# Kernel optimization log

Measured on AMD Instinct MI355X. Metric: run time of the kernel, lower is better.

The kernel has to match this reference:

```python
import jax, jax.numpy as jnp
import numpy as np

N, D_IN, D_HID, P, D_OUT = 131072, 256, 256, 256, 2


def setup_inputs() -> dict:
    key = jax.random.key(0)
    ks = jax.random.split(key, 10)
    s_in = 1.0 / np.sqrt(D_IN)
    s_h = 1.0 / np.sqrt(D_HID)
    s_o = 1.0 / np.sqrt(P)
    return {
        "X_batch": jax.random.normal(ks[0], (N, D_IN), dtype=jnp.float32),
        "W_in": jax.random.uniform(ks[1], (D_HID, D_IN), jnp.float32, -s_in, s_in),
        "b_in": jax.random.uniform(ks[2], (D_HID,), jnp.float32, -s_in, s_in),
        "W_h1": jax.random.uniform(ks[3], (D_HID, D_HID), jnp.float32, -s_h, s_h),
        "b_h1": jax.random.uniform(ks[4], (D_HID,), jnp.float32, -s_h, s_h),
        "W_h2": jax.random.uniform(ks[5], (D_HID, D_HID), jnp.float32, -s_h, s_h),
        "b_h2": jax.random.uniform(ks[6], (D_HID,), jnp.float32, -s_h, s_h),
        "prototype": jax.random.normal(ks[7], (P, D_HID), dtype=jnp.float32),
        "W_out": jax.random.uniform(ks[8], (D_OUT, P), jnp.float32, -s_o, s_o),
        "b_out": jax.random.uniform(ks[9], (D_OUT,), jnp.float32, -s_o, s_o),
        "assignment": 0,
    }


def reference(X_batch, W_in, b_in, W_h1, b_h1, W_h2, b_h2, prototype, W_out, b_out, assignment):
    # forward_a: fc_in + relu, then hidden layers + relu
    h = jax.nn.relu(X_batch @ W_in.T + b_in)          # (N, d)
    h = jax.nn.relu(h @ W_h1.T + b_h1)
    h = jax.nn.relu(h @ W_h2.T + b_h2)
    # forward_prototype: L2-normalize hidden and prototypes, then inner product.
    hn = h / jnp.linalg.norm(h, axis=1, keepdims=True)                      # (N, d)
    pn = prototype / jnp.linalg.norm(prototype, axis=1, keepdims=True)      # (p, d)
    # FAITHFUL to torch: .view(1, d, p) is a row-major RESHAPE of (p, d),
    # not a transpose. The broadcast mul+sum reduces to a single GEMM.
    d, p = hn.shape[1], pn.shape[0]
    proto_mat = pn.reshape(d, p)                                            # (d, p)
    inner = hn @ proto_mat                                                  # (N, p)
    return inner @ W_out.T + b_out                                          # (N, out)
```

## Files before the change

kernel.cpp:

```cpp
#include <hip/hip_runtime.h>
#include <hip/hip_bf16.h>

#define DHID 256
#define ROWS 64
#define THREADS 512
#define NROWS 131072

typedef __attribute__((ext_vector_type(8))) __bf16 bf16x8;
typedef __attribute__((ext_vector_type(4))) float f32x4;

__device__ __forceinline__ unsigned short f2b(float f) {
    union { float f; unsigned u; } x; x.f = f;
    unsigned r = x.u + 0x7fffu + ((x.u >> 16) & 1u);
    return (unsigned short)(r >> 16);
}

__device__ __forceinline__ int hswz(int row, int col) {
    return ((row << 9) + (col << 1)) ^ ((row & 7) << 4);
}

__global__ void conv_w(const float* __restrict__ w0, const float* __restrict__ w1,
                       const float* __restrict__ w2, unsigned short* __restrict__ out) {
    int i = blockIdx.x * blockDim.x + threadIdx.x;
    const float* src = (i < 65536) ? w0 : (i < 131072 ? w1 : w2);
    int rem  = i & 65535;
    int e    = rem & 7;
    int lane = (rem >> 3) & 63;
    int blk  = rem >> 9;
    int kk   = blk & 7;
    int c16  = blk >> 3;
    int row  = c16 * 16 + (lane & 15);
    int col  = kk * 32 + 8 * (lane >> 4) + e;
    out[i] = f2b(src[row * 256 + col]);
}

__global__ void make_m(const float* __restrict__ proto, const float* __restrict__ wout,
                       float2* __restrict__ M) {
    int k = blockIdx.x;
    int l = threadIdx.x;
    float s2 = 0.f, d0 = 0.f, d1 = 0.f;
#pragma unroll
    for (int q = 0; q < 4; ++q) {
        int c = l + 64 * q;
        float p = proto[k * 256 + c];
        s2 += p * p;
        d0 += p * wout[c];
        d1 += p * wout[256 + c];
    }
#pragma unroll
    for (int off = 32; off; off >>= 1) {
        s2 += __shfl_xor(s2, off);
        d0 += __shfl_xor(d0, off);
        d1 += __shfl_xor(d1, off);
    }
    if (l == 0) {
        float rinv = rsqrtf(s2);
        M[k] = make_float2(d0 * rinv, d1 * rinv);
    }
}

__device__ __forceinline__ void layer(const unsigned short* hin, unsigned short* hout,
                                      const unsigned short* W, const float* __restrict__ bias,
                                      int lane, int wave) {
    const int l15 = lane & 15;
    const int g   = lane >> 4;
    const int jw  = wave * 32;

    f32x4 acc[4][2];
#pragma unroll
    for (int ci = 0; ci < 2; ++ci) {
        const float4 bv = *reinterpret_cast<const float4*>(&bias[jw + 16 * ci + 4 * g]);
#pragma unroll
        for (int ri = 0; ri < 4; ++ri) {
            acc[ri][ci][0] = bv.x; acc[ri][ci][1] = bv.y;
            acc[ri][ci][2] = bv.z; acc[ri][ci][3] = bv.w;
        }
    }

    const char* hin_b = reinterpret_cast<const char*>(hin);
    const unsigned short* wp[2];
#pragma unroll
    for (int ci = 0; ci < 2; ++ci)
        wp[ci] = W + ((wave * 2 + ci) * 8) * 512 + lane * 8;

    bf16x8 bcur[2];
#pragma unroll
    for (int ci = 0; ci < 2; ++ci) bcur[ci] = *reinterpret_cast<const bf16x8*>(wp[ci]);

#pragma unroll
    for (int kk = 0; kk < 8; ++kk) {
        const int k0 = kk * 32 + 8 * g;
        bf16x8 a[4];
#pragma unroll
        for (int ri = 0; ri < 4; ++ri)
            a[ri] = *reinterpret_cast<const bf16x8*>(hin_b + hswz(16 * ri + l15, k0));
        bf16x8 bnxt[2];
        if (kk < 7) {
#pragma unroll
            for (int ci = 0; ci < 2; ++ci)
                bnxt[ci] = *reinterpret_cast<const bf16x8*>(wp[ci] + (kk + 1) * 512);
        }
#pragma unroll
        for (int ri = 0; ri < 4; ++ri)
#pragma unroll
            for (int ci = 0; ci < 2; ++ci)
                acc[ri][ci] = __builtin_amdgcn_mfma_f32_16x16x32_bf16(bcur[ci], a[ri], acc[ri][ci], 0, 0, 0);
        if (kk < 7) { bcur[0] = bnxt[0]; bcur[1] = bnxt[1]; }
    }

    char* hout_b = reinterpret_cast<char*>(hout);
#pragma unroll
    for (int ri = 0; ri < 4; ++ri) {
        const int row = 16 * ri + l15;
#pragma unroll
        for (int ci = 0; ci < 2; ++ci) {
            const int colb = jw + 16 * ci + 4 * g;
            unsigned long long pk =
                  (unsigned long long)f2b(fmaxf(acc[ri][ci][0], 0.f))
                | ((unsigned long long)f2b(fmaxf(acc[ri][ci][1], 0.f)) << 16)
                | ((unsigned long long)f2b(fmaxf(acc[ri][ci][2], 0.f)) << 32)
                | ((unsigned long long)f2b(fmaxf(acc[ri][ci][3], 0.f)) << 48);
            *reinterpret_cast<unsigned long long*>(hout_b + hswz(row, colb)) = pk;
        }
    }
}

__device__ __forceinline__ void layer3_reduce(const unsigned short* hin,
                                              const unsigned short* W,
                                              const float* __restrict__ bias,
                                              const float2* __restrict__ M,
                                              float* part, int lane, int wave) {
    const int l15 = lane & 15;
    const int g   = lane >> 4;
    const int jw  = wave * 32;

    f32x4 acc[4][2];
#pragma unroll
    for (int ci = 0; ci < 2; ++ci) {
        const float4 bv = *reinterpret_cast<const float4*>(&bias[jw + 16 * ci + 4 * g]);
#pragma unroll
        for (int ri = 0; ri < 4; ++ri) {
            acc[ri][ci][0] = bv.x; acc[ri][ci][1] = bv.y;
            acc[ri][ci][2] = bv.z; acc[ri][ci][3] = bv.w;
        }
    }

    const char* hin_b = reinterpret_cast<const char*>(hin);
    const unsigned short* wp[2];
#pragma unroll
    for (int ci = 0; ci < 2; ++ci)
        wp[ci] = W + ((wave * 2 + ci) * 8) * 512 + lane * 8;

    bf16x8 bcur[2];
#pragma unroll
    for (int ci = 0; ci < 2; ++ci) bcur[ci] = *reinterpret_cast<const bf16x8*>(wp[ci]);

#pragma unroll
    for (int kk = 0; kk < 8; ++kk) {
        const int k0 = kk * 32 + 8 * g;
        bf16x8 a[4];
#pragma unroll
        for (int ri = 0; ri < 4; ++ri)
            a[ri] = *reinterpret_cast<const bf16x8*>(hin_b + hswz(16 * ri + l15, k0));
        bf16x8 bnxt[2];
        if (kk < 7) {
#pragma unroll
            for (int ci = 0; ci < 2; ++ci)
                bnxt[ci] = *reinterpret_cast<const bf16x8*>(wp[ci] + (kk + 1) * 512);
        }
#pragma unroll
        for (int ri = 0; ri < 4; ++ri)
#pragma unroll
            for (int ci = 0; ci < 2; ++ci)
                acc[ri][ci] = __builtin_amdgcn_mfma_f32_16x16x32_bf16(bcur[ci], a[ri], acc[ri][ci], 0, 0, 0);
        if (kk < 7) { bcur[0] = bnxt[0]; bcur[1] = bnxt[1]; }
    }

    float2 m[2][4];
#pragma unroll
    for (int ci = 0; ci < 2; ++ci)
#pragma unroll
        for (int e = 0; e < 4; ++e)
            m[ci][e] = M[jw + 16 * ci + 4 * g + e];

    float s2[4], d0[4], d1[4];
#pragma unroll
    for (int ri = 0; ri < 4; ++ri) {
        s2[ri] = 0.f; d0[ri] = 0.f; d1[ri] = 0.f;
#pragma unroll
        for (int ci = 0; ci < 2; ++ci)
#pragma unroll
            for (int e = 0; e < 4; ++e) {
                float h = fmaxf(acc[ri][ci][e], 0.f);
                s2[ri] += h * h;
                d0[ri] += h * m[ci][e].x;
                d1[ri] += h * m[ci][e].y;
            }
    }
#pragma unroll
    for (int ri = 0; ri < 4; ++ri) {
        s2[ri] += __shfl_xor(s2[ri], 16); s2[ri] += __shfl_xor(s2[ri], 32);
        d0[ri] += __shfl_xor(d0[ri], 16); d0[ri] += __shfl_xor(d0[ri], 32);
        d1[ri] += __shfl_xor(d1[ri], 16); d1[ri] += __shfl_xor(d1[ri], 32);
    }
    if (lane < 16) {
#pragma unroll
        for (int ri = 0; ri < 4; ++ri) {
            int r = 16 * ri + l15;
            part[r * 8 + wave]        = s2[ri];
            part[512 + r * 8 + wave]  = d0[ri];
            part[1024 + r * 8 + wave] = d1[ri];
        }
    }
}

__global__ __launch_bounds__(THREADS, 4) void mlp_fused(
    const float* __restrict__ X,
    const unsigned short* __restrict__ Wb,
    const float* __restrict__ b0,
    const float* __restrict__ b1,
    const float* __restrict__ b2,
    const float2* __restrict__ M,
    const float* __restrict__ bout,
    float* __restrict__ out)
{
    __shared__ unsigned short hbuf[2][ROWS * DHID];

    const int tid  = threadIdx.x;
    const int lane = tid & 63;
    const int wave = tid >> 6;
    const int row0 = blockIdx.x * ROWS;

#pragma unroll
    for (int it = 0; it < 8; ++it) {
        int idx = tid + (it << 9);
        int r = idx >> 6;
        int c = (idx & 63) << 2;
        const float4 v = *reinterpret_cast<const float4*>(X + (size_t)(row0 + r) * DHID + c);
        unsigned long long pk =
              (unsigned long long)f2b(v.x)
            | ((unsigned long long)f2b(v.y) << 16)
            | ((unsigned long long)f2b(v.z) << 32)
            | ((unsigned long long)f2b(v.w) << 48);
        *reinterpret_cast<unsigned long long*>(reinterpret_cast<char*>(&hbuf[0][0]) + hswz(r, c)) = pk;
    }
    __syncthreads();

    layer(&hbuf[0][0], &hbuf[1][0], Wb,             b0, lane, wave);
    __syncthreads();
    layer(&hbuf[1][0], &hbuf[0][0], Wb + 65536,     b1, lane, wave);
    __syncthreads();
    float* part = reinterpret_cast<float*>(&hbuf[1][0]);
    layer3_reduce(&hbuf[0][0], Wb + 2 * 65536, b2, M, part, lane, wave);
    __syncthreads();

    if (tid < 128) {
        int r = tid >> 1, dsel = tid & 1;
        float s = 0.f, dd = 0.f;
        const float* ps = part + r * 8;
        const float* pd = part + 512 + dsel * 512 + r * 8;
#pragma unroll
        for (int w = 0; w < 8; ++w) { s += ps[w]; dd += pd[w]; }
        out[(size_t)(row0 + r) * 2 + dsel] = dd * rsqrtf(s) + bout[dsel];
    }
}

extern "C" void kernel_launch(void* const* d_in, const int* in_sizes, int n_in,
                              void* d_out, int out_size, void* d_ws, size_t ws_size,
                              hipStream_t stream) {
    const float* X     = (const float*)d_in[0];
    const float* W_in  = (const float*)d_in[1];
    const float* b_in  = (const float*)d_in[2];
    const float* W_h1  = (const float*)d_in[3];
    const float* b_h1  = (const float*)d_in[4];
    const float* W_h2  = (const float*)d_in[5];
    const float* b_h2  = (const float*)d_in[6];
    const float* proto = (const float*)d_in[7];
    const float* W_out = (const float*)d_in[8];
    const float* b_out = (const float*)d_in[9];

    unsigned short* Wb = (unsigned short*)d_ws;
    float2*         M  = (float2*)((char*)d_ws + 3 * 65536 * 2);
    float*          out = (float*)d_out;

    conv_w<<<768, 256, 0, stream>>>(W_in, W_h1, W_h2, Wb);
    make_m<<<256, 64, 0, stream>>>(proto, W_out, M);
    mlp_fused<<<NROWS / ROWS, THREADS, 0, stream>>>(X, Wb, b_in, b_h1, b_h2, M, b_out, out);
}
```

Measured before the change: 77.70 us.

## Halve waves per block and widen per-wave output tile with deeper weight prefetch

Cuts the block to 4 waves, each computing a 64-column slice (4 MFMA column tiles) instead of 32, so each LDS A-fragment read is reused across twice as many MFMAs. Weight fragments are now prefetched two k-steps ahead with a ping-pong register buffer. The partial-sum layout and final reduction are resized for 4 waves. This raises register pressure (16 accumulators plus 8 B fragments) and lowers the launch-bounds occupancy hint to 2 blocks, which risks less latency hiding.

After: 80.44 us. 1.04x slower.

```diff
diff --git a/kernel.cpp b/kernel.cpp
--- a/kernel.cpp
+++ b/kernel.cpp
@@ -3,7 +3,7 @@
 
 #define DHID 256
 #define ROWS 64
-#define THREADS 512
+#define THREADS 256
 #define NROWS 131072
 
 typedef __attribute__((ext_vector_type(8))) __bf16 bf16x8;
@@ -64,11 +64,11 @@
                                       int lane, int wave) {
     const int l15 = lane & 15;
     const int g   = lane >> 4;
-    const int jw  = wave * 32;
-
-    f32x4 acc[4][2];
-#pragma unroll
-    for (int ci = 0; ci < 2; ++ci) {
+    const int jw  = wave * 64;
+
+    f32x4 acc[4][4];
+#pragma unroll
+    for (int ci = 0; ci < 4; ++ci) {
         const float4 bv = *reinterpret_cast<const float4*>(&bias[jw + 16 * ci + 4 * g]);
 #pragma unroll
         for (int ri = 0; ri < 4; ++ri) {
@@ -78,14 +78,16 @@
     }
 
     const char* hin_b = reinterpret_cast<const char*>(hin);
-    const unsigned short* wp[2];
-#pragma unroll
-    for (int ci = 0; ci < 2; ++ci)
-        wp[ci] = W + ((wave * 2 + ci) * 8) * 512 + lane * 8;
-
-    bf16x8 bcur[2];
-#pragma unroll
-    for (int ci = 0; ci < 2; ++ci) bcur[ci] = *reinterpret_cast<const bf16x8*>(wp[ci]);
+    const unsigned short* wp[4];
+#pragma unroll
+    for (int ci = 0; ci < 4; ++ci)
+        wp[ci] = W + ((wave * 4 + ci) * 8) * 512 + lane * 8;
+
+    bf16x8 bq0[4], bq1[4];
+#pragma unroll
+    for (int ci = 0; ci < 4; ++ci) bq0[ci] = *reinterpret_cast<const bf16x8*>(wp[ci]);
+#pragma unroll
+    for (int ci = 0; ci < 4; ++ci) bq1[ci] = *reinterpret_cast<const bf16x8*>(wp[ci] + 512);
 
 #pragma unroll
     for (int kk = 0; kk < 8; ++kk) {
@@ -94,18 +96,25 @@
 #pragma unroll
         for (int ri = 0; ri < 4; ++ri)
             a[ri] = *reinterpret_cast<const bf16x8*>(hin_b + hswz(16 * ri + l15, k0));
-        bf16x8 bnxt[2];
-        if (kk < 7) {
-#pragma unroll
-            for (int ci = 0; ci < 2; ++ci)
-                bnxt[ci] = *reinterpret_cast<const bf16x8*>(wp[ci] + (kk + 1) * 512);
+        bf16x8 bn[4];
+        if (kk < 6) {
+#pragma unroll
+            for (int ci = 0; ci < 4; ++ci)
+                bn[ci] = *reinterpret_cast<const bf16x8*>(wp[ci] + (kk + 2) * 512);
         }
 #pragma unroll
         for (int ri = 0; ri < 4; ++ri)
 #pragma unroll
-            for (int ci = 0; ci < 2; ++ci)
-                acc[ri][ci] = __builtin_amdgcn_mfma_f32_16x16x32_bf16(bcur[ci], a[ri], acc[ri][ci], 0, 0, 0);
-        if (kk < 7) { bcur[0] = bnxt[0]; bcur[1] = bnxt[1]; }
+            for (int ci = 0; ci < 4; ++ci) {
+                bf16x8 bu = (kk & 1) ? bq1[ci] : bq0[ci];
+                acc[ri][ci] = __builtin_amdgcn_mfma_f32_16x16x32_bf16(bu, a[ri], acc[ri][ci], 0, 0, 0);
+            }
+        if (kk < 6) {
+#pragma unroll
+            for (int ci = 0; ci < 4; ++ci) {
+                if (kk & 1) bq1[ci] = bn[ci]; else bq0[ci] = bn[ci];
+            }
+        }
     }
 
     char* hout_b = reinterpret_cast<char*>(hout);
@@ -113,7 +122,7 @@
     for (int ri = 0; ri < 4; ++ri) {
         const int row = 16 * ri + l15;
 #pragma unroll
-        for (int ci = 0; ci < 2; ++ci) {
+        for (int ci = 0; ci < 4; ++ci) {
             const int colb = jw + 16 * ci + 4 * g;
             unsigned long long pk =
                   (unsigned long long)f2b(fmaxf(acc[ri][ci][0], 0.f))
@@ -132,11 +141,11 @@
                                               float* part, int lane, int wave) {
     const int l15 = lane & 15;
     const int g   = lane >> 4;
-    const int jw  = wave * 32;
-
-    f32x4 acc[4][2];
-#pragma unroll
-    for (int ci = 0; ci < 2; ++ci) {
+    const int jw  = wave * 64;
+
+    f32x4 acc[4][4];
+#pragma unroll
+    for (int ci = 0; ci < 4; ++ci) {
         const float4 bv = *reinterpret_cast<const float4*>(&bias[jw + 16 * ci + 4 * g]);
 #pragma unroll
         for (int ri = 0; ri < 4; ++ri) {
@@ -146,14 +155,16 @@
     }
 
     const char* hin_b = reinterpret_cast<const char*>(hin);
-    const unsigned short* wp[2];
-#pragma unroll
-    for (int ci = 0; ci < 2; ++ci)
-        wp[ci] = W + ((wave * 2 + ci) * 8) * 512 + lane * 8;
-
-    bf16x8 bcur[2];
-#pragma unroll
-    for (int ci = 0; ci < 2; ++ci) bcur[ci] = *reinterpret_cast<const bf16x8*>(wp[ci]);
+    const unsigned short* wp[4];
+#pragma unroll
+    for (int ci = 0; ci < 4; ++ci)
+        wp[ci] = W + ((wave * 4 + ci) * 8) * 512 + lane * 8;
+
+    bf16x8 bq0[4], bq1[4];
+#pragma unroll
+    for (int ci = 0; ci < 4; ++ci) bq0[ci] = *reinterpret_cast<const bf16x8*>(wp[ci]);
+#pragma unroll
+    for (int ci = 0; ci < 4; ++ci) bq1[ci] = *reinterpret_cast<const bf16x8*>(wp[ci] + 512);
 
 #pragma unroll
     for (int kk = 0; kk < 8; ++kk) {
@@ -162,23 +173,30 @@
 #pragma unroll
         for (int ri = 0; ri < 4; ++ri)
             a[ri] = *reinterpret_cast<const bf16x8*>(hin_b + hswz(16 * ri + l15, k0));
-        bf16x8 bnxt[2];
-        if (kk < 7) {
-#pragma unroll
-            for (int ci = 0; ci < 2; ++ci)
-                bnxt[ci] = *reinterpret_cast<const bf16x8*>(wp[ci] + (kk + 1) * 512);
+        bf16x8 bn[4];
+        if (kk < 6) {
+#pragma unroll
+            for (int ci = 0; ci < 4; ++ci)
+                bn[ci] = *reinterpret_cast<const bf16x8*>(wp[ci] + (kk + 2) * 512);
         }
 #pragma unroll
         for (int ri = 0; ri < 4; ++ri)
 #pragma unroll
-            for (int ci = 0; ci < 2; ++ci)
-                acc[ri][ci] = __builtin_amdgcn_mfma_f32_16x16x32_bf16(bcur[ci], a[ri], acc[ri][ci], 0, 0, 0);
-        if (kk < 7) { bcur[0] = bnxt[0]; bcur[1] = bnxt[1]; }
-    }
-
-    float2 m[2][4];
-#pragma unroll
-    for (int ci = 0; ci < 2; ++ci)
+            for (int ci = 0; ci < 4; ++ci) {
+                bf16x8 bu = (kk & 1) ? bq1[ci] : bq0[ci];
+                acc[ri][ci] = __builtin_amdgcn_mfma_f32_16x16x32_bf16(bu, a[ri], acc[ri][ci], 0, 0, 0);
+            }
+        if (kk < 6) {
+#pragma unroll
+            for (int ci = 0; ci < 4; ++ci) {
+                if (kk & 1) bq1[ci] = bn[ci]; else bq0[ci] = bn[ci];
+            }
+        }
+    }
+
+    float2 m[4][4];
+#pragma unroll
+    for (int ci = 0; ci < 4; ++ci)
 #pragma unroll
         for (int e = 0; e < 4; ++e)
             m[ci][e] = M[jw + 16 * ci + 4 * g + e];
@@ -188,7 +206,7 @@
     for (int ri = 0; ri < 4; ++ri) {
         s2[ri] = 0.f; d0[ri] = 0.f; d1[ri] = 0.f;
 #pragma unroll
-        for (int ci = 0; ci < 2; ++ci)
+        for (int ci = 0; ci < 4; ++ci)
 #pragma unroll
             for (int e = 0; e < 4; ++e) {
                 float h = fmaxf(acc[ri][ci][e], 0.f);
@@ -207,14 +225,14 @@
 #pragma unroll
         for (int ri = 0; ri < 4; ++ri) {
             int r = 16 * ri + l15;
-            part[r * 8 + wave]        = s2[ri];
-            part[512 + r * 8 + wave]  = d0[ri];
-            part[1024 + r * 8 + wave] = d1[ri];
-        }
-    }
-}
-
-__global__ __launch_bounds__(THREADS, 4) void mlp_fused(
+            part[r * 4 + wave]        = s2[ri];
+            part[256 + r * 4 + wave]  = d0[ri];
+            part[512 + r * 4 + wave]  = d1[ri];
+        }
+    }
+}
+
+__global__ __launch_bounds__(THREADS, 2) void mlp_fused(
     const float* __restrict__ X,
     const unsigned short* __restrict__ Wb,
     const float* __restrict__ b0,
@@ -232,8 +250,8 @@
     const int row0 = blockIdx.x * ROWS;
 
 #pragma unroll
-    for (int it = 0; it < 8; ++it) {
-        int idx = tid + (it << 9);
+    for (int it = 0; it < 16; ++it) {
+        int idx = tid + (it << 8);
         int r = idx >> 6;
         int c = (idx & 63) << 2;
         const float4 v = *reinterpret_cast<const float4*>(X + (size_t)(row0 + r) * DHID + c);
@@ -257,10 +275,10 @@
     if (tid < 128) {
         int r = tid >> 1, dsel = tid & 1;
         float s = 0.f, dd = 0.f;
-        const float* ps = part + r * 8;
-        const float* pd = part + 512 + dsel * 512 + r * 8;
-#pragma unroll
-        for (int w = 0; w < 8; ++w) { s += ps[w]; dd += pd[w]; }
+        const float* ps = part + r * 4;
+        const float* pd = part + 256 + dsel * 256 + r * 4;
+#pragma unroll
+        for (int w = 0; w < 4; ++w) { s += ps[w]; dd += pd[w]; }
         out[(size_t)(row0 + r) * 2 + dsel] = dd * rsqrtf(s) + bout[dsel];
     }
 }
```
